# Kernel optimization log

Hardware: AMD Instinct MI355X
Metric: run time of the kernel (lower is better)

Reference implementation:

```python
import jax, jax.numpy as jnp
import numpy as np


def setup_inputs() -> dict:
    key = jax.random.key(0)
    k1, k2, k3, k4 = jax.random.split(key, 4)
    B, C, H, W = 8, 64, 64, 64
    Ck = C // 8  # query/key channels
    x = jax.random.normal(k1, (B, C, H, W), dtype=jnp.float32)
    # 1x1 conv1d weights (bias=False); spectral norm only rescales the weight,
    # so plain matrices are math-equivalent at a given parameter value.
    wq = jax.random.normal(k2, (Ck, C), dtype=jnp.float32) * (1.0 / np.sqrt(C))
    wk = jax.random.normal(k3, (Ck, C), dtype=jnp.float32) * (1.0 / np.sqrt(C))
    wv = jax.random.normal(k4, (C, C), dtype=jnp.float32) * (1.0 / np.sqrt(C))
    gamma = jnp.array([0.5], dtype=jnp.float32)  # nonzero so attention path is exercised
    return {"x": x, "wq": wq, "wk": wk, "wv": wv, "gamma": gamma}


def reference(x, wq, wk, wv, gamma):
    B, C, H, W = x.shape
    xf = x.reshape(B, C, H * W)                      # [B, C, N]
    f = jnp.einsum('kc,bcn->bkn', wq, xf)            # [B, C/8, N]
    g = jnp.einsum('kc,bcn->bkn', wk, xf)            # [B, C/8, N]
    h = jnp.einsum('oc,bcn->bon', wv, xf)            # [B, C,   N]
    scores = jnp.einsum('bkn,bkm->bnm', f, g)        # f^T g, [B, N, N]
    beta = jax.nn.softmax(scores, axis=1)            # softmax over dim=1 (rows), as in torch
    o = jnp.einsum('bcn,bnm->bcm', h, beta)          # [B, C, N]
    out = gamma[0] * o + xf
    return out.reshape(B, C, H, W)
```

## Files before the change

### kernel.cpp

```cpp
#include <hip/hip_runtime.h>
#include <hip/hip_bf16.h>

typedef __bf16 bf16x8 __attribute__((ext_vector_type(8)));
typedef float f32x4 __attribute__((ext_vector_type(4)));
typedef float f32x16 __attribute__((ext_vector_type(16)));

#define MFMA16 __builtin_amdgcn_mfma_f32_16x16x32_bf16
#define MFMA32 __builtin_amdgcn_mfma_f32_32x32x16_bf16

__device__ __forceinline__ unsigned short f2b(float f) {
  unsigned int u = __float_as_uint(f);
  u += 0x7FFFu + ((u >> 16) & 1u);
  return (unsigned short)(u >> 16);
}

__device__ __forceinline__ float b2f(unsigned short s) {
  return __uint_as_float(((unsigned)s) << 16);
}

union U128 {
  uint4 u;
  unsigned short s[8];
  bf16x8 b;
};

union BPack {
  __hip_bfloat162 h2;
  unsigned u;
};

__device__ __forceinline__ unsigned packbf(float a, float b) {
  BPack p;
  p.h2 = __float22bfloat162_rn(make_float2(a, b));
  return p.u;
}

__global__ __launch_bounds__(256, 2) void proj_kernel(
    const float* __restrict__ x, const float* __restrict__ wq,
    const float* __restrict__ wk, const float* __restrict__ wv_w,
    unsigned short* __restrict__ f_t, unsigned short* __restrict__ g_t,
    unsigned short* __restrict__ h_out) {
  __shared__ unsigned short xT[64 * 64];
  __shared__ unsigned short wT[96 * 72];

  const int tid = (int)threadIdx.x;
  const int wvp = tid >> 6;
  const int lane = tid & 63;
  const int b = (int)blockIdx.x & 7;
  const int n0 = ((int)blockIdx.x >> 3) << 6;

  {
    const float* xb = x + ((size_t)b << 18) + n0 + lane;
    const int c0 = wvp * 16;
    float xv[16];
#pragma unroll
    for (int cc = 0; cc < 16; ++cc) xv[cc] = xb[(size_t)(c0 + cc) << 12];
#pragma unroll
    for (int p = 0; p < 4; ++p) {
      const int c = c0 + 4 * p;
      uint2 d;
      d.x = packbf(xv[4 * p + 0], xv[4 * p + 1]);
      d.y = packbf(xv[4 * p + 2], xv[4 * p + 3]);
      const int g = c >> 3;
      const int idx = lane * 64 + (((g ^ (lane & 7)) << 3) | (((c >> 2) & 1) << 2));
      *(uint2*)&xT[idx] = d;
    }
  }
#pragma unroll
  for (int i = 0; i < 20; ++i) {
    const int idx = i * 256 + tid;
    const float wval = (idx < 512) ? wq[idx] * 1.44269504f
                     : (idx < 1024) ? wk[idx - 512]
                                    : wv_w[idx - 1024];
    wT[(idx >> 6) * 72 + (idx & 63)] = f2b(wval);
  }
  __syncthreads();

  const int t = lane & 15, q = lane >> 4;
  const int nloc = wvp * 16 + t;
  U128 Bf[2];
#pragma unroll
  for (int kp = 0; kp < 2; ++kp) {
    const int g = kp * 4 + q;
    Bf[kp].u = *(const uint4*)&xT[nloc * 64 + ((g ^ (nloc & 7)) << 3)];
  }
  const int nabs = n0 + nloc;
#pragma unroll
  for (int rt = 0; rt < 5; ++rt) {
    f32x4 acc = {0.f, 0.f, 0.f, 0.f};
#pragma unroll
    for (int kp = 0; kp < 2; ++kp) {
      U128 Af;
      Af.u = *(const uint4*)&wT[(rt * 16 + t) * 72 + ((kp * 4 + q) << 3)];
      acc = MFMA16(Af.b, Bf[kp].b, acc, 0, 0, 0);
    }
#pragma unroll
    for (int reg = 0; reg < 4; ++reg) {
      const int r = rt * 16 + 4 * q + reg;
      const unsigned short v = f2b(acc[reg]);
      if (r < 8)
        f_t[((size_t)((b << 12) + nabs) << 3) + r] = v;
      else if (r < 16)
        g_t[((size_t)((b << 12) + nabs) << 3) + (r - 8)] = v;
      else
        h_out[((size_t)b << 18) + ((size_t)(nabs >> 3) << 9) +
              ((r - 16) << 3) + (nabs & 7)] = v;
    }
  }
}

__global__ __launch_bounds__(256, 6) void attn_kernel(
    const unsigned short* __restrict__ f_t, const unsigned short* __restrict__ g_t,
    const unsigned short* __restrict__ h, const float* __restrict__ x,
    const float* __restrict__ gamma, float* __restrict__ out) {
  __shared__ unsigned short Opart[4][32][66];
  __shared__ float lred[4][32];
  __shared__ float lsum[32];

  const int tid = (int)threadIdx.x;
  const int wave = tid >> 6;
  const int lane = tid & 63;
  const int ml = lane & 31;
  const int hh = lane >> 5;

  const int b = (int)blockIdx.x & 7;
  const int m32 = ((int)blockIdx.x >> 3) << 5;

  const unsigned short* fb = f_t + ((size_t)b << 15);
  const unsigned short* hb = h + ((size_t)b << 18);

  U128 G;
  G.u = make_uint4(0u, 0u, 0u, 0u);
  if (hh == 0) G.u = *(const uint4*)(g_t + ((size_t)((b << 12) + m32 + ml) << 3));

  f32x16 O0 = {}, O1 = {};
  float lpa = 0.f, lpb = 0.f;

  const int nbase = wave << 10;
  U128 F;
  F.u = *(const uint4*)(fb + ((size_t)(nbase + ml) << 3));

  for (int it = 0; it < 32; ++it) {
    const int n32 = nbase + (it << 5);

    U128 H00, H01, H10, H11;
    {
      const unsigned short* hg = hb + ((n32 >> 3) << 9) + (hh << 9) + (ml << 3);
      H00.u = *(const uint4*)(hg);
      H10.u = *(const uint4*)(hg + 256);
      H01.u = *(const uint4*)(hg + 1024);
      H11.u = *(const uint4*)(hg + 1024 + 256);
    }
    U128 Fn = F;
    if (it < 31)
      Fn.u = *(const uint4*)(fb + ((size_t)(n32 + 32 + ml) << 3));

    const f32x16 z = {};
    f32x16 S = MFMA32(F.b, G.b, z, 0, 0, 0);
    F = Fn;

    float e[16];
#pragma unroll
    for (int r = 0; r < 16; ++r) e[r] = __builtin_amdgcn_exp2f(S[r]);
#pragma unroll
    for (int r = 0; r < 8; ++r) {
      lpa += e[2 * r];
      lpb += e[2 * r + 1];
    }

#pragma unroll
    for (int kt = 0; kt < 2; ++kt) {
      const unsigned A0 = packbf(e[8 * kt + 0], e[8 * kt + 1]);
      const unsigned A1 = packbf(e[8 * kt + 2], e[8 * kt + 3]);
      const unsigned B0 = packbf(e[8 * kt + 4], e[8 * kt + 5]);
      const unsigned B1 = packbf(e[8 * kt + 6], e[8 * kt + 7]);
      const unsigned s0 = hh ? A0 : B0;
      const unsigned s1 = hh ? A1 : B1;
      const unsigned r0 = (unsigned)__shfl_xor((int)s0, 32, 64);
      const unsigned r1 = (unsigned)__shfl_xor((int)s1, 32, 64);
      U128 P;
      P.u.x = hh ? r0 : A0;
      P.u.y = hh ? r1 : A1;
      P.u.z = hh ? B0 : r0;
      P.u.w = hh ? B1 : r1;
      if (kt == 0) {
        O0 = MFMA32(H00.b, P.b, O0, 0, 0, 0);
        O1 = MFMA32(H10.b, P.b, O1, 0, 0, 0);
      } else {
        O0 = MFMA32(H01.b, P.b, O0, 0, 0, 0);
        O1 = MFMA32(H11.b, P.b, O1, 0, 0, 0);
      }
    }
  }

  float lp = lpa + lpb;
  lp += __shfl_xor(lp, 32, 64);
  if (hh == 0) lred[wave][ml] = lp;
#pragma unroll
  for (int r = 0; r < 8; ++r) {
    const int c0 = ((2 * r) & 3) + 8 * (r >> 1) + 4 * hh;
    *(unsigned*)&Opart[wave][ml][c0] = packbf(O0[2 * r], O0[2 * r + 1]);
    *(unsigned*)&Opart[wave][ml][c0 + 32] = packbf(O1[2 * r], O1[2 * r + 1]);
  }
  __syncthreads();
  if (tid < 32)
    lsum[tid] = (lred[0][tid] + lred[1][tid]) + (lred[2][tid] + lred[3][tid]);
  __syncthreads();

  const int c = tid >> 2;
  const int m0l = (tid & 3) << 3;
  const float gam = gamma[0];
  float a[8];
#pragma unroll
  for (int j = 0; j < 8; ++j) a[j] = 0.f;
#pragma unroll
  for (int w = 0; w < 4; ++w)
#pragma unroll
    for (int j = 0; j < 8; ++j) a[j] += b2f(Opart[w][m0l + j][c]);

  const f32x4 l0 = *(const f32x4*)&lsum[m0l];
  const f32x4 l1 = *(const f32x4*)&lsum[m0l + 4];
  const size_t oi = (((size_t)b * 64 + c) << 12) + m32 + m0l;
  f32x4 xo0 = *(const f32x4*)(x + oi);
  f32x4 xo1 = *(const f32x4*)(x + oi + 4);
#pragma unroll
  for (int j = 0; j < 4; ++j) {
    xo0[j] += gam / l0[j] * a[j];
    xo1[j] += gam / l1[j] * a[j + 4];
  }
  *(f32x4*)(out + oi) = xo0;
  *(f32x4*)(out + oi + 4) = xo1;
}

extern "C" void kernel_launch(void* const* d_in, const int* in_sizes, int n_in,
                              void* d_out, int out_size, void* d_ws, size_t ws_size,
                              hipStream_t stream) {
  (void)in_sizes; (void)n_in; (void)out_size; (void)ws_size;
  const float* x = (const float*)d_in[0];
  const float* wq = (const float*)d_in[1];
  const float* wk = (const float*)d_in[2];
  const float* wv = (const float*)d_in[3];
  const float* gamma = (const float*)d_in[4];
  float* out = (float*)d_out;

  unsigned short* f_t = (unsigned short*)d_ws;
  unsigned short* g_t = f_t + (size_t)8 * 4096 * 8;
  unsigned short* h = g_t + (size_t)8 * 4096 * 8;

  proj_kernel<<<512, 256, 0, stream>>>(x, wq, wk, wv, f_t, g_t, h);
  attn_kernel<<<1024, 256, 0, stream>>>(f_t, g_t, h, x, gamma, out);
}
```

Before: 109.0 us.

## Process 64 query columns per attention block with 8 waves sharing H loads

```diff
diff --git a/kernel.cpp b/kernel.cpp
--- a/kernel.cpp
+++ b/kernel.cpp
@@ -109,13 +109,13 @@
   }
 }
 
-__global__ __launch_bounds__(256, 6) void attn_kernel(
+__global__ __launch_bounds__(512, 4) void attn_kernel(
     const unsigned short* __restrict__ f_t, const unsigned short* __restrict__ g_t,
     const unsigned short* __restrict__ h, const float* __restrict__ x,
     const float* __restrict__ gamma, float* __restrict__ out) {
-  __shared__ unsigned short Opart[4][32][66];
-  __shared__ float lred[4][32];
-  __shared__ float lsum[32];
+  __shared__ unsigned short Opart[8][64][66];
+  __shared__ float lred[8][64];
+  __shared__ float lsum[64];
 
   const int tid = (int)threadIdx.x;
   const int wave = tid >> 6;
@@ -124,23 +124,25 @@
   const int hh = lane >> 5;
 
   const int b = (int)blockIdx.x & 7;
-  const int m32 = ((int)blockIdx.x >> 3) << 5;
+  const int m64 = ((int)blockIdx.x >> 3) << 6;
 
   const unsigned short* fb = f_t + ((size_t)b << 15);
   const unsigned short* hb = h + ((size_t)b << 18);
 
-  U128 G;
-  G.u = make_uint4(0u, 0u, 0u, 0u);
-  if (hh == 0) G.u = *(const uint4*)(g_t + ((size_t)((b << 12) + m32 + ml) << 3));
-
-  f32x16 O0 = {}, O1 = {};
-  float lpa = 0.f, lpb = 0.f;
-
-  const int nbase = wave << 10;
-  U128 F;
-  F.u = *(const uint4*)(fb + ((size_t)(nbase + ml) << 3));
-
-  for (int it = 0; it < 32; ++it) {
+  U128 GA, GB;
+  GA.u = make_uint4(0u, 0u, 0u, 0u);
+  GB.u = make_uint4(0u, 0u, 0u, 0u);
+  if (hh == 0) {
+    GA.u = *(const uint4*)(g_t + ((size_t)((b << 12) + m64 + ml) << 3));
+    GB.u = *(const uint4*)(g_t + ((size_t)((b << 12) + m64 + 32 + ml) << 3));
+  }
+
+  f32x16 OA0 = {}, OA1 = {}, OB0 = {}, OB1 = {};
+  float lpA = 0.f, lpB = 0.f;
+
+  const int nbase = wave << 9;
+
+  for (int it = 0; it < 16; ++it) {
     const int n32 = nbase + (it << 5);
 
     U128 H00, H01, H10, H11;
@@ -151,29 +153,24 @@
       H01.u = *(const uint4*)(hg + 1024);
       H11.u = *(const uint4*)(hg + 1024 + 256);
     }
-    U128 Fn = F;
-    if (it < 31)
-      Fn.u = *(const uint4*)(fb + ((size_t)(n32 + 32 + ml) << 3));
+    U128 F;
+    F.u = *(const uint4*)(fb + ((size_t)(n32 + ml) << 3));
 
     const f32x16 z = {};
-    f32x16 S = MFMA32(F.b, G.b, z, 0, 0, 0);
-    F = Fn;
-
-    float e[16];
-#pragma unroll
-    for (int r = 0; r < 16; ++r) e[r] = __builtin_amdgcn_exp2f(S[r]);
-#pragma unroll
-    for (int r = 0; r < 8; ++r) {
-      lpa += e[2 * r];
-      lpb += e[2 * r + 1];
-    }
+    f32x16 SA = MFMA32(F.b, GA.b, z, 0, 0, 0);
+    f32x16 SB = MFMA32(F.b, GB.b, z, 0, 0, 0);
 
 #pragma unroll
     for (int kt = 0; kt < 2; ++kt) {
-      const unsigned A0 = packbf(e[8 * kt + 0], e[8 * kt + 1]);
-      const unsigned A1 = packbf(e[8 * kt + 2], e[8 * kt + 3]);
-      const unsigned B0 = packbf(e[8 * kt + 4], e[8 * kt + 5]);
-      const unsigned B1 = packbf(e[8 * kt + 6], e[8 * kt + 7]);
+      float e[8];
+#pragma unroll
+      for (int r = 0; r < 8; ++r) e[r] = __builtin_amdgcn_exp2f(SA[8 * kt + r]);
+#pragma unroll
+      for (int r = 0; r < 8; ++r) lpA += e[r];
+      const unsigned A0 = packbf(e[0], e[1]);
+      const unsigned A1 = packbf(e[2], e[3]);
+      const unsigned B0 = packbf(e[4], e[5]);
+      const unsigned B1 = packbf(e[6], e[7]);
       const unsigned s0 = hh ? A0 : B0;
       const unsigned s1 = hh ? A1 : B1;
       const unsigned r0 = (unsigned)__shfl_xor((int)s0, 32, 64);
@@ -184,43 +181,81 @@
       P.u.z = hh ? B0 : r0;
       P.u.w = hh ? B1 : r1;
       if (kt == 0) {
-        O0 = MFMA32(H00.b, P.b, O0, 0, 0, 0);
-        O1 = MFMA32(H10.b, P.b, O1, 0, 0, 0);
+        OA0 = MFMA32(H00.b, P.b, OA0, 0, 0, 0);
+        OA1 = MFMA32(H10.b, P.b, OA1, 0, 0, 0);
       } else {
-        O0 = MFMA32(H01.b, P.b, O0, 0, 0, 0);
-        O1 = MFMA32(H11.b, P.b, O1, 0, 0, 0);
+        OA0 = MFMA32(H01.b, P.b, OA0, 0, 0, 0);
+        OA1 = MFMA32(H11.b, P.b, OA1, 0, 0, 0);
       }
     }
-  }
-
-  float lp = lpa + lpb;
-  lp += __shfl_xor(lp, 32, 64);
-  if (hh == 0) lred[wave][ml] = lp;
+
+#pragma unroll
+    for (int kt = 0; kt < 2; ++kt) {
+      float e[8];
+#pragma unroll
+      for (int r = 0; r < 8; ++r) e[r] = __builtin_amdgcn_exp2f(SB[8 * kt + r]);
+#pragma unroll
+      for (int r = 0; r < 8; ++r) lpB += e[r];
+      const unsigned A0 = packbf(e[0], e[1]);
+      const unsigned A1 = packbf(e[2], e[3]);
+      const unsigned B0 = packbf(e[4], e[5]);
+      const unsigned B1 = packbf(e[6], e[7]);
+      const unsigned s0 = hh ? A0 : B0;
+      const unsigned s1 = hh ? A1 : B1;
+      const unsigned r0 = (unsigned)__shfl_xor((int)s0, 32, 64);
+      const unsigned r1 = (unsigned)__shfl_xor((int)s1, 32, 64);
+      U128 P;
+      P.u.x = hh ? r0 : A0;
+      P.u.y = hh ? r1 : A1;
+      P.u.z = hh ? B0 : r0;
+      P.u.w = hh ? B1 : r1;
+      if (kt == 0) {
+        OB0 = MFMA32(H00.b, P.b, OB0, 0, 0, 0);
+        OB1 = MFMA32(H10.b, P.b, OB1, 0, 0, 0);
+      } else {
+        OB0 = MFMA32(H01.b, P.b, OB0, 0, 0, 0);
+        OB1 = MFMA32(H11.b, P.b, OB1, 0, 0, 0);
+      }
+    }
+  }
+
+  lpA += __shfl_xor(lpA, 32, 64);
+  lpB += __shfl_xor(lpB, 32, 64);
+  if (hh == 0) {
+    lred[wave][ml] = lpA;
+    lred[wave][32 + ml] = lpB;
+  }
 #pragma unroll
   for (int r = 0; r < 8; ++r) {
     const int c0 = ((2 * r) & 3) + 8 * (r >> 1) + 4 * hh;
-    *(unsigned*)&Opart[wave][ml][c0] = packbf(O0[2 * r], O0[2 * r + 1]);
-    *(unsigned*)&Opart[wave][ml][c0 + 32] = packbf(O1[2 * r], O1[2 * r + 1]);
+    *(unsigned*)&Opart[wave][ml][c0] = packbf(OA0[2 * r], OA0[2 * r + 1]);
+    *(unsigned*)&Opart[wave][ml][c0 + 32] = packbf(OA1[2 * r], OA1[2 * r + 1]);
+    *(unsigned*)&Opart[wave][32 + ml][c0] = packbf(OB0[2 * r], OB0[2 * r + 1]);
+    *(unsigned*)&Opart[wave][32 + ml][c0 + 32] = packbf(OB1[2 * r], OB1[2 * r + 1]);
   }
   __syncthreads();
-  if (tid < 32)
-    lsum[tid] = (lred[0][tid] + lred[1][tid]) + (lred[2][tid] + lred[3][tid]);
+  if (tid < 64) {
+    float s = 0.f;
+#pragma unroll
+    for (int w = 0; w < 8; ++w) s += lred[w][tid];
+    lsum[tid] = s;
+  }
   __syncthreads();
 
-  const int c = tid >> 2;
-  const int m0l = (tid & 3) << 3;
+  const int c = tid >> 3;
+  const int m0l = (tid & 7) << 3;
   const float gam = gamma[0];
   float a[8];
 #pragma unroll
   for (int j = 0; j < 8; ++j) a[j] = 0.f;
 #pragma unroll
-  for (int w = 0; w < 4; ++w)
+  for (int w = 0; w < 8; ++w)
 #pragma unroll
     for (int j = 0; j < 8; ++j) a[j] += b2f(Opart[w][m0l + j][c]);
 
   const f32x4 l0 = *(const f32x4*)&lsum[m0l];
   const f32x4 l1 = *(const f32x4*)&lsum[m0l + 4];
-  const size_t oi = (((size_t)b * 64 + c) << 12) + m32 + m0l;
+  const size_t oi = (((size_t)b * 64 + c) << 12) + m64 + m0l;
   f32x4 xo0 = *(const f32x4*)(x + oi);
   f32x4 xo1 = *(const f32x4*)(x + oi + 4);
 #pragma unroll
@@ -248,5 +283,5 @@
   unsigned short* h = g_t + (size_t)8 * 4096 * 8;
 
   proj_kernel<<<512, 256, 0, stream>>>(x, wq, wk, wv, f_t, g_t, h);
-  attn_kernel<<<1024, 256, 0, stream>>>(f_t, g_t, h, x, gamma, out);
-}
+  attn_kernel<<<512, 512, 0, stream>>>(f_t, g_t, h, x, gamma, out);
+}
```

Result: slower. 122.9 us (+12.8%).

## Switch attention kernel to 16x16 MFMA tiles with 16-query blocks

Applied to the files above, without the earlier changes.

```diff
diff --git a/kernel.cpp b/kernel.cpp
--- a/kernel.cpp
+++ b/kernel.cpp
@@ -3,10 +3,8 @@
 
 typedef __bf16 bf16x8 __attribute__((ext_vector_type(8)));
 typedef float f32x4 __attribute__((ext_vector_type(4)));
-typedef float f32x16 __attribute__((ext_vector_type(16)));
 
 #define MFMA16 __builtin_amdgcn_mfma_f32_16x16x32_bf16
-#define MFMA32 __builtin_amdgcn_mfma_f32_32x32x16_bf16
 
 __device__ __forceinline__ unsigned short f2b(float f) {
   unsigned int u = __float_as_uint(f);
@@ -113,123 +111,122 @@
     const unsigned short* __restrict__ f_t, const unsigned short* __restrict__ g_t,
     const unsigned short* __restrict__ h, const float* __restrict__ x,
     const float* __restrict__ gamma, float* __restrict__ out) {
-  __shared__ unsigned short Opart[4][32][66];
-  __shared__ float lred[4][32];
-  __shared__ float lsum[32];
+  __shared__ unsigned short Opart[4][16][66];
+  __shared__ float lred[4][16];
+  __shared__ float lsum[16];
 
   const int tid = (int)threadIdx.x;
   const int wave = tid >> 6;
   const int lane = tid & 63;
-  const int ml = lane & 31;
+  const int t = lane & 15;
+  const int q = lane >> 4;
   const int hh = lane >> 5;
 
   const int b = (int)blockIdx.x & 7;
-  const int m32 = ((int)blockIdx.x >> 3) << 5;
+  const int m0 = ((int)blockIdx.x >> 3) << 4;
 
   const unsigned short* fb = f_t + ((size_t)b << 15);
   const unsigned short* hb = h + ((size_t)b << 18);
 
   U128 G;
   G.u = make_uint4(0u, 0u, 0u, 0u);
-  if (hh == 0) G.u = *(const uint4*)(g_t + ((size_t)((b << 12) + m32 + ml) << 3));
-
-  f32x16 O0 = {}, O1 = {};
-  float lpa = 0.f, lpb = 0.f;
+  if (q == 0) G.u = *(const uint4*)(g_t + ((size_t)((b << 12) + m0 + t) << 3));
+
+  f32x4 O0 = {}, O1 = {}, O2 = {}, O3 = {};
+  float lp = 0.f;
+
+  const int bpa = (t + (((q & 1) << 1) << 4)) << 2;
+  const int bpb = bpa + 64;
 
   const int nbase = wave << 10;
-  U128 F;
-  F.u = *(const uint4*)(fb + ((size_t)(nbase + ml) << 3));
 
   for (int it = 0; it < 32; ++it) {
     const int n32 = nbase + (it << 5);
 
-    U128 H00, H01, H10, H11;
-    {
-      const unsigned short* hg = hb + ((n32 >> 3) << 9) + (hh << 9) + (ml << 3);
-      H00.u = *(const uint4*)(hg);
-      H10.u = *(const uint4*)(hg + 256);
-      H01.u = *(const uint4*)(hg + 1024);
-      H11.u = *(const uint4*)(hg + 1024 + 256);
-    }
-    U128 Fn = F;
-    if (it < 31)
-      Fn.u = *(const uint4*)(fb + ((size_t)(n32 + 32 + ml) << 3));
-
-    const f32x16 z = {};
-    f32x16 S = MFMA32(F.b, G.b, z, 0, 0, 0);
-    F = Fn;
-
-    float e[16];
-#pragma unroll
-    for (int r = 0; r < 16; ++r) e[r] = __builtin_amdgcn_exp2f(S[r]);
-#pragma unroll
-    for (int r = 0; r < 8; ++r) {
-      lpa += e[2 * r];
-      lpb += e[2 * r + 1];
-    }
-
-#pragma unroll
-    for (int kt = 0; kt < 2; ++kt) {
-      const unsigned A0 = packbf(e[8 * kt + 0], e[8 * kt + 1]);
-      const unsigned A1 = packbf(e[8 * kt + 2], e[8 * kt + 3]);
-      const unsigned B0 = packbf(e[8 * kt + 4], e[8 * kt + 5]);
-      const unsigned B1 = packbf(e[8 * kt + 6], e[8 * kt + 7]);
-      const unsigned s0 = hh ? A0 : B0;
-      const unsigned s1 = hh ? A1 : B1;
-      const unsigned r0 = (unsigned)__shfl_xor((int)s0, 32, 64);
-      const unsigned r1 = (unsigned)__shfl_xor((int)s1, 32, 64);
-      U128 P;
-      P.u.x = hh ? r0 : A0;
-      P.u.y = hh ? r1 : A1;
-      P.u.z = hh ? B0 : r0;
-      P.u.w = hh ? B1 : r1;
-      if (kt == 0) {
-        O0 = MFMA32(H00.b, P.b, O0, 0, 0, 0);
-        O1 = MFMA32(H10.b, P.b, O1, 0, 0, 0);
-      } else {
-        O0 = MFMA32(H01.b, P.b, O0, 0, 0, 0);
-        O1 = MFMA32(H11.b, P.b, O1, 0, 0, 0);
-      }
-    }
-  }
-
-  float lp = lpa + lpb;
+    const unsigned short* hg = hb + ((size_t)n32 << 6) + (q << 9) + (t << 3);
+    U128 H0, H1, H2, H3;
+    H0.u = *(const uint4*)(hg);
+    H1.u = *(const uint4*)(hg + 128);
+    H2.u = *(const uint4*)(hg + 256);
+    H3.u = *(const uint4*)(hg + 384);
+
+    U128 F0, F1;
+    F0.u = *(const uint4*)(fb + ((size_t)(n32 + t) << 3));
+    F1.u = *(const uint4*)(fb + ((size_t)(n32 + 16 + t) << 3));
+
+    const f32x4 z4 = {0.f, 0.f, 0.f, 0.f};
+    f32x4 S0 = MFMA16(F0.b, G.b, z4, 0, 0, 0);
+    f32x4 S1 = MFMA16(F1.b, G.b, z4, 0, 0, 0);
+
+    float e0 = __builtin_amdgcn_exp2f(S0[0]);
+    float e1 = __builtin_amdgcn_exp2f(S0[1]);
+    float e2 = __builtin_amdgcn_exp2f(S0[2]);
+    float e3 = __builtin_amdgcn_exp2f(S0[3]);
+    float e4 = __builtin_amdgcn_exp2f(S1[0]);
+    float e5 = __builtin_amdgcn_exp2f(S1[1]);
+    float e6 = __builtin_amdgcn_exp2f(S1[2]);
+    float e7 = __builtin_amdgcn_exp2f(S1[3]);
+    lp += ((e0 + e1) + (e2 + e3)) + ((e4 + e5) + (e6 + e7));
+
+    const int d00 = (int)packbf(e0, e1);
+    const int d01 = (int)packbf(e2, e3);
+    const int d10 = (int)packbf(e4, e5);
+    const int d11 = (int)packbf(e6, e7);
+
+    const int p0a = __builtin_amdgcn_ds_bpermute(bpa, d00);
+    const int p0b = __builtin_amdgcn_ds_bpermute(bpa, d01);
+    const int p0c = __builtin_amdgcn_ds_bpermute(bpb, d00);
+    const int p0d = __builtin_amdgcn_ds_bpermute(bpb, d01);
+    const int p1a = __builtin_amdgcn_ds_bpermute(bpa, d10);
+    const int p1b = __builtin_amdgcn_ds_bpermute(bpa, d11);
+    const int p1c = __builtin_amdgcn_ds_bpermute(bpb, d10);
+    const int p1d = __builtin_amdgcn_ds_bpermute(bpb, d11);
+
+    U128 P;
+    P.u.x = (unsigned)(hh ? p1a : p0a);
+    P.u.y = (unsigned)(hh ? p1b : p0b);
+    P.u.z = (unsigned)(hh ? p1c : p0c);
+    P.u.w = (unsigned)(hh ? p1d : p0d);
+
+    O0 = MFMA16(H0.b, P.b, O0, 0, 0, 0);
+    O1 = MFMA16(H1.b, P.b, O1, 0, 0, 0);
+    O2 = MFMA16(H2.b, P.b, O2, 0, 0, 0);
+    O3 = MFMA16(H3.b, P.b, O3, 0, 0, 0);
+  }
+
+  lp += __shfl_xor(lp, 16, 64);
   lp += __shfl_xor(lp, 32, 64);
-  if (hh == 0) lred[wave][ml] = lp;
-#pragma unroll
-  for (int r = 0; r < 8; ++r) {
-    const int c0 = ((2 * r) & 3) + 8 * (r >> 1) + 4 * hh;
-    *(unsigned*)&Opart[wave][ml][c0] = packbf(O0[2 * r], O0[2 * r + 1]);
-    *(unsigned*)&Opart[wave][ml][c0 + 32] = packbf(O1[2 * r], O1[2 * r + 1]);
+  if (lane < 16) lred[wave][t] = lp;
+
+#pragma unroll
+  for (int ct = 0; ct < 4; ++ct) {
+    const f32x4 Ov = (ct == 0) ? O0 : (ct == 1) ? O1 : (ct == 2) ? O2 : O3;
+    const int cb = 16 * ct + 4 * q;
+    *(unsigned*)&Opart[wave][t][cb] = packbf(Ov[0], Ov[1]);
+    *(unsigned*)&Opart[wave][t][cb + 2] = packbf(Ov[2], Ov[3]);
   }
   __syncthreads();
-  if (tid < 32)
+  if (tid < 16)
     lsum[tid] = (lred[0][tid] + lred[1][tid]) + (lred[2][tid] + lred[3][tid]);
   __syncthreads();
 
   const int c = tid >> 2;
-  const int m0l = (tid & 3) << 3;
+  const int ms = (tid & 3) << 2;
   const float gam = gamma[0];
-  float a[8];
-#pragma unroll
-  for (int j = 0; j < 8; ++j) a[j] = 0.f;
+  float a[4];
+#pragma unroll
+  for (int j = 0; j < 4; ++j) a[j] = 0.f;
 #pragma unroll
   for (int w = 0; w < 4; ++w)
 #pragma unroll
-    for (int j = 0; j < 8; ++j) a[j] += b2f(Opart[w][m0l + j][c]);
-
-  const f32x4 l0 = *(const f32x4*)&lsum[m0l];
-  const f32x4 l1 = *(const f32x4*)&lsum[m0l + 4];
-  const size_t oi = (((size_t)b * 64 + c) << 12) + m32 + m0l;
-  f32x4 xo0 = *(const f32x4*)(x + oi);
-  f32x4 xo1 = *(const f32x4*)(x + oi + 4);
-#pragma unroll
-  for (int j = 0; j < 4; ++j) {
-    xo0[j] += gam / l0[j] * a[j];
-    xo1[j] += gam / l1[j] * a[j + 4];
-  }
-  *(f32x4*)(out + oi) = xo0;
-  *(f32x4*)(out + oi + 4) = xo1;
+    for (int j = 0; j < 4; ++j) a[j] += b2f(Opart[w][ms + j][c]);
+
+  const f32x4 lv = *(const f32x4*)&lsum[ms];
+  const size_t oi = (((size_t)b * 64 + c) << 12) + m0 + ms;
+  f32x4 xo = *(const f32x4*)(x + oi);
+#pragma unroll
+  for (int j = 0; j < 4; ++j) xo[j] += gam / lv[j] * a[j];
+  *(f32x4*)(out + oi) = xo;
 }
 
 extern "C" void kernel_launch(void* const* d_in, const int* in_sizes, int n_in,
@@ -248,5 +245,5 @@
   unsigned short* h = g_t + (size_t)8 * 4096 * 8;
 
   proj_kernel<<<512, 256, 0, stream>>>(x, wq, wk, wv, f_t, g_t, h);
-  attn_kernel<<<1024, 256, 0, stream>>>(f_t, g_t, h, x, gamma, out);
-}
+  attn_kernel<<<2048, 256, 0, stream>>>(f_t, g_t, h, x, gamma, out);
+}
```

Measured after the change: 121.5 us. 11.4% more time.
